# Kernel optimization log

Measured on AMD Instinct MI355X. Metric: run time of the kernel, lower is better.

The kernel has to match this reference:

```python
import jax, jax.numpy as jnp
import numpy as np

N_NODES = 50000
D_IN = 128
D_OUT = 128
E_POS = 500000
E_NEG = 100000
BN_EPS = 1e-5


def setup_inputs() -> dict:
    key = jax.random.key(0)
    k = jax.random.split(key, 4)
    x = jax.random.normal(k[0], (N_NODES, D_IN), dtype=jnp.float32)
    pos_edge_index = jax.random.randint(k[1], (2, E_POS), 0, N_NODES, dtype=jnp.int64)
    neg_edge_index = jax.random.randint(k[2], (2, E_NEG), 0, N_NODES, dtype=jnp.int64)
    W = jax.random.normal(k[3], (D_IN, D_OUT), dtype=jnp.float32) * 0.05
    b = jnp.zeros((D_OUT,), dtype=jnp.float32)
    gamma = jnp.ones((D_OUT,), dtype=jnp.float32)
    beta = jnp.zeros((D_OUT,), dtype=jnp.float32)
    return {"x": x, "pos_edge_index": pos_edge_index, "neg_edge_index": neg_edge_index,
            "W": W, "b": b, "gamma": gamma, "beta": beta}


def reference(x, pos_edge_index, neg_edge_index, W, b, gamma, beta):
    N = x.shape[0]
    # edge weights: 1 for pos edges, 0 for neg edges (as in the torch module)
    ei = jnp.concatenate([pos_edge_index, neg_edge_index], axis=1)
    w = jnp.concatenate([jnp.ones((pos_edge_index.shape[1],), x.dtype),
                         jnp.zeros((neg_edge_index.shape[1],), x.dtype)])
    # GCNConv gcn_norm: add self-loops with weight 1.0
    loop = jnp.arange(N)
    row = jnp.concatenate([ei[0], loop])
    col = jnp.concatenate([ei[1], loop])
    w = jnp.concatenate([w, jnp.ones((N,), x.dtype)])
    # symmetric degree normalization over target (col)
    deg = jax.ops.segment_sum(w, col, num_segments=N)
    dis = jnp.where(deg > 0, jax.lax.rsqrt(jnp.maximum(deg, 1e-12)), 0.0)
    norm = dis[row] * w * dis[col]  # [E_total]
    # linear transform first, then scatter-add aggregation at col
    h = x @ W  # [N, D_OUT]
    out = jax.ops.segment_sum(norm[:, None] * h[row], col, num_segments=N) + b
    # BatchNorm1d (training mode, biased batch var) + ReLU
    mean = out.mean(axis=0)
    var = out.var(axis=0)
    xhat = (out - mean) * jax.lax.rsqrt(var + BN_EPS)
    return jax.nn.relu(gamma * xhat + beta)
```

## Files before the change

### kernel.cpp

```cpp
#include <hip/hip_runtime.h>

#define D 128
#define BN_EPS 1e-5f
#define K_ELL 40
#define NB_AGG 1024

typedef __attribute__((ext_vector_type(8))) short bf16x8;
typedef __attribute__((ext_vector_type(4))) float f32x4;

__device__ __forceinline__ unsigned bf16rne(float f) {
    unsigned u = __float_as_uint(f);
    return (u + 0x7fffu + ((u >> 16) & 1u)) >> 16;
}
__device__ __forceinline__ float bflo(unsigned p) { return __uint_as_float(p << 16); }
__device__ __forceinline__ float bfhi(unsigned p) { return __uint_as_float(p & 0xffff0000u); }

__global__ void prep(const int* __restrict__ prow, const int* __restrict__ pcol,
                     int* __restrict__ deg, int* __restrict__ ell,
                     int2* __restrict__ ovf, int* __restrict__ ovf_cnt,
                     const float* __restrict__ W, ushort* __restrict__ wbT, int E) {
    int gtid = blockIdx.x * blockDim.x + threadIdx.x;
    int gsz = gridDim.x * blockDim.x;
    for (int i = gtid; i < D * D; i += gsz) {
        int k = i >> 7, c = i & 127;
        wbT[c * D + k] = (ushort)bf16rne(W[i]);
    }
    for (int e = gtid; e < E; e += gsz) {
        int c = pcol[e];
        int r = prow[e];
        int p = atomicAdd(&deg[c], 1);
        if (p < K_ELL) {
            ell[c * K_ELL + p] = r;
        } else {
            int q = atomicAdd(ovf_cnt, 1);
            ovf[q] = make_int2(c, r);
        }
    }
}

__global__ __launch_bounds__(256) void gemm_mfma(const float* __restrict__ x,
                                                 const ushort* __restrict__ wbT,
                                                 ushort* __restrict__ hb, int n) {
    __shared__ ushort xsb[64][136];
    __shared__ ushort wsb[128][136];
    int tid = threadIdx.x;
    int wave = tid >> 6;
    int lane = tid & 63;
    int row0 = blockIdx.x * 64;

    #pragma unroll
    for (int i = 0; i < 8; i++) {
        int flat = i * 256 + tid;
        int c = flat >> 4, seg = flat & 15;
        *(uint4*)&wsb[c][seg * 8] = ((const uint4*)wbT)[flat];
    }
    {
        int r = tid >> 2, kq = tid & 3;
        int grow = row0 + r;
        if (grow >= n) grow = n - 1;
        const float4* src = (const float4*)&x[(size_t)grow * D + kq * 32];
        uint* dst = (uint*)&xsb[r][kq * 32];
        #pragma unroll
        for (int q = 0; q < 8; q++) {
            float4 v = src[q];
            dst[q * 2]     = bf16rne(v.x) | (bf16rne(v.y) << 16);
            dst[q * 2 + 1] = bf16rne(v.z) | (bf16rne(v.w) << 16);
        }
    }
    __syncthreads();

    f32x4 acc[4][2];
    #pragma unroll
    for (int mt = 0; mt < 4; mt++)
        #pragma unroll
        for (int nt = 0; nt < 2; nt++)
            acc[mt][nt] = (f32x4){0.f, 0.f, 0.f, 0.f};

    int ar = lane & 15;
    int ako = (lane >> 4) * 8;
    #pragma unroll
    for (int k0 = 0; k0 < 128; k0 += 32) {
        bf16x8 a[4], b[2];
        #pragma unroll
        for (int mt = 0; mt < 4; mt++)
            a[mt] = *(const bf16x8*)&xsb[mt * 16 + ar][k0 + ako];
        #pragma unroll
        for (int nt = 0; nt < 2; nt++)
            b[nt] = *(const bf16x8*)&wsb[wave * 32 + nt * 16 + ar][k0 + ako];
        #pragma unroll
        for (int mt = 0; mt < 4; mt++)
            #pragma unroll
            for (int nt = 0; nt < 2; nt++)
                acc[mt][nt] = __builtin_amdgcn_mfma_f32_16x16x32_bf16(
                    a[mt], b[nt], acc[mt][nt], 0, 0, 0);
    }

    int col = lane & 15, rq = (lane >> 4) * 4;
    #pragma unroll
    for (int mt = 0; mt < 4; mt++) {
        #pragma unroll
        for (int r = 0; r < 4; r++) {
            int grow = row0 + mt * 16 + rq + r;
            if (grow < n) {
                #pragma unroll
                for (int nt = 0; nt < 2; nt++)
                    hb[(size_t)grow * D + wave * 32 + nt * 16 + col] =
                        (ushort)bf16rne(acc[mt][nt][r]);
            }
        }
    }
}

__global__ __launch_bounds__(512) void aggregate(const unsigned* __restrict__ hb,
                                                 const int* __restrict__ deg,
                                                 const int* __restrict__ ell,
                                                 const int2* __restrict__ ovf,
                                                 const int* __restrict__ ovf_cnt,
                                                 const float* __restrict__ bias,
                                                 float* __restrict__ out,
                                                 float* __restrict__ partials, int n) {
    int tid = threadIdx.x;
    int wave = tid >> 6;
    int lane = tid & 63;
    float2 bv = *(const float2*)&bias[lane * 2];
    float s1a = 0.f, s1b = 0.f, s2a = 0.f, s2b = 0.f;

    for (int node = blockIdx.x * 8 + wave; node < n; node += gridDim.x * 8) {
        int cntT = deg[node];
        float dc = rsqrtf((float)cntT + 1.0f);
        int cntE = cntT < K_ELL ? cntT : K_ELL;
        unsigned hp = hb[(size_t)node * 64 + lane];
        float ax = dc * bflo(hp), ay = dc * bfhi(hp);
        int es = (lane < cntE) ? ell[node * K_ELL + lane] : 0;
        float ed = (lane < cntE) ? rsqrtf((float)deg[es] + 1.0f) : 0.f;
        int e = 0;
        for (; e + 4 <= cntE; e += 4) {
            int sA = __shfl(es, e), sB = __shfl(es, e + 1);
            int sC = __shfl(es, e + 2), sD = __shfl(es, e + 3);
            float dA = __shfl(ed, e), dB = __shfl(ed, e + 1);
            float dC = __shfl(ed, e + 2), dD = __shfl(ed, e + 3);
            unsigned hA = hb[(size_t)sA * 64 + lane];
            unsigned hB = hb[(size_t)sB * 64 + lane];
            unsigned hC = hb[(size_t)sC * 64 + lane];
            unsigned hD = hb[(size_t)sD * 64 + lane];
            ax += dA * bflo(hA); ay += dA * bfhi(hA);
            ax += dB * bflo(hB); ay += dB * bfhi(hB);
            ax += dC * bflo(hC); ay += dC * bfhi(hC);
            ax += dD * bflo(hD); ay += dD * bfhi(hD);
        }
        for (; e < cntE; e++) {
            int s = __shfl(es, e);
            float dv = __shfl(ed, e);
            unsigned hq = hb[(size_t)s * 64 + lane];
            ax += dv * bflo(hq); ay += dv * bfhi(hq);
        }
        if (cntT > K_ELL) {
            int novf = *ovf_cnt;
            for (int j = 0; j < novf; j++) {
                int2 q = ovf[j];
                if (q.x == node) {
                    float dv = rsqrtf((float)deg[q.y] + 1.0f);
                    unsigned hq = hb[(size_t)q.y * 64 + lane];
                    ax += dv * bflo(hq); ay += dv * bfhi(hq);
                }
            }
        }
        float ox = dc * ax + bv.x;
        float oy = dc * ay + bv.y;
        *(float2*)&out[(size_t)node * D + lane * 2] = make_float2(ox, oy);
        s1a += ox; s1b += oy;
        s2a += ox * ox; s2b += oy * oy;
    }

    __shared__ float l1[8][128], l2[8][128];
    l1[wave][lane * 2] = s1a; l1[wave][lane * 2 + 1] = s1b;
    l2[wave][lane * 2] = s2a; l2[wave][lane * 2 + 1] = s2b;
    __syncthreads();
    if (tid < 256) {
        int col = tid & 127;
        float v;
        if (tid < 128) {
            v = l1[0][col] + l1[1][col] + l1[2][col] + l1[3][col] +
                l1[4][col] + l1[5][col] + l1[6][col] + l1[7][col];
        } else {
            v = l2[0][col] + l2[1][col] + l2[2][col] + l2[3][col] +
                l2[4][col] + l2[5][col] + l2[6][col] + l2[7][col];
        }
        partials[(size_t)blockIdx.x * 256 + tid] = v;
    }
}

__global__ __launch_bounds__(256) void bn_reduce(const float* __restrict__ partials,
                                                 float* __restrict__ gsum,
                                                 float* __restrict__ gsumsq, int nrows) {
    int tid = threadIdx.x;
    float s = 0.f;
    for (int r = blockIdx.x; r < nrows; r += gridDim.x)
        s += partials[(size_t)r * 256 + tid];
    if (tid < 128) atomicAdd(&gsum[tid], s);
    else           atomicAdd(&gsumsq[tid - 128], s);
}

__global__ __launch_bounds__(256) void bn_finalize(float4* __restrict__ out4,
                                                   const float* __restrict__ gsum,
                                                   const float* __restrict__ gsumsq,
                                                   const float* __restrict__ gamma,
                                                   const float* __restrict__ beta,
                                                   int total4, float invN) {
    int i0 = blockIdx.x * 256 + threadIdx.x;
    int c = (i0 * 4) & 127;
    float4 g4 = *(const float4*)&gsum[c];
    float4 q4 = *(const float4*)&gsumsq[c];
    float4 gm = *(const float4*)&gamma[c];
    float4 bt = *(const float4*)&beta[c];
    float m0 = g4.x * invN, m1 = g4.y * invN, m2 = g4.z * invN, m3 = g4.w * invN;
    float sc0 = rsqrtf(q4.x * invN - m0 * m0 + BN_EPS) * gm.x;
    float sc1 = rsqrtf(q4.y * invN - m1 * m1 + BN_EPS) * gm.y;
    float sc2 = rsqrtf(q4.z * invN - m2 * m2 + BN_EPS) * gm.z;
    float sc3 = rsqrtf(q4.w * invN - m3 * m3 + BN_EPS) * gm.w;
    float sh0 = bt.x - m0 * sc0, sh1 = bt.y - m1 * sc1;
    float sh2 = bt.z - m2 * sc2, sh3 = bt.w - m3 * sc3;
    for (int i = i0; i < total4; i += gridDim.x * 256) {
        float4 v = out4[i];
        v.x = fmaxf(fmaf(v.x, sc0, sh0), 0.f);
        v.y = fmaxf(fmaf(v.y, sc1, sh1), 0.f);
        v.z = fmaxf(fmaf(v.z, sc2, sh2), 0.f);
        v.w = fmaxf(fmaf(v.w, sc3, sh3), 0.f);
        out4[i] = v;
    }
}

extern "C" void kernel_launch(void* const* d_in, const int* in_sizes, int n_in,
                              void* d_out, int out_size, void* d_ws, size_t ws_size,
                              hipStream_t stream) {
    const float* x     = (const float*)d_in[0];
    const int*   pos   = (const int*)d_in[1];
    const float* W     = (const float*)d_in[3];
    const float* bias  = (const float*)d_in[4];
    const float* gamma = (const float*)d_in[5];
    const float* beta  = (const float*)d_in[6];
    float* out = (float*)d_out;

    int N  = in_sizes[0] / D;
    int EP = in_sizes[1] / 2;
    const int* prow = pos;
    const int* pcol = pos + EP;

    auto align = [](size_t v) { return (v + 255) & ~(size_t)255; };
    char* p = (char*)d_ws;
    int*      deg     = (int*)p;      p += align((size_t)N * 4);
    int*      ovf_cnt = (int*)p;      p += align(256);
    float*    gsum    = (float*)p;    p += align((size_t)D * 4);
    float*    gsumsq  = (float*)p;    p += align((size_t)D * 4);
    size_t zbytes = (size_t)(p - (char*)d_ws);
    ushort*   wbT      = (ushort*)p;   p += align((size_t)D * D * 2);
    int*      ell      = (int*)p;      p += align((size_t)N * K_ELL * 4);
    int2*     ovf      = (int2*)p;     p += align((size_t)EP * 8);
    ushort*   hb       = (ushort*)p;   p += align((size_t)N * D * 2);
    float*    partials = (float*)p;    p += align((size_t)NB_AGG * 256 * 4);

    hipMemsetAsync(d_ws, 0, zbytes, stream);
    prep<<<(EP + 255) / 256, 256, 0, stream>>>(prow, pcol, deg, ell, ovf, ovf_cnt,
                                               W, wbT, EP);
    gemm_mfma<<<(N + 63) / 64, 256, 0, stream>>>(x, wbT, hb, N);
    aggregate<<<NB_AGG, 512, 0, stream>>>((const unsigned*)hb, deg, ell, ovf, ovf_cnt,
                                          bias, out, partials, N);
    bn_reduce<<<64, 256, 0, stream>>>(partials, gsum, gsumsq, NB_AGG);
    bn_finalize<<<1600, 256, 0, stream>>>((float4*)out, gsum, gsumsq, gamma, beta,
                                          N * D / 4, 1.0f / (float)N);
}
```

Before: 158.7 us.

## Fuse GEMM with ELL fill, process two nodes per wave, fold BN reduce into aggregate

Merges the edge-bucketing prep kernel into the GEMM launch as extra blocks, so the GEMM converts W to bf16 directly instead of reading a pre-transposed copy. Aggregation now handles two nodes per wave, using half-waves to hold neighbor lists and issuing eight gathers per iteration for more memory-level parallelism. The separate BN reduction kernel is replaced by a last-block ticket reduction inside aggregate that writes per-column scale and shift. This removes two launches and overlaps the GEMM with the atomic fill, at the cost of redundant W conversion per GEMM block and more divergence and register pressure in aggregation.

Result: slower. 570.4 us (+259.5%).

```diff
diff --git a/kernel.cpp b/kernel.cpp
--- a/kernel.cpp
+++ b/kernel.cpp
@@ -4,6 +4,7 @@
 #define BN_EPS 1e-5f
 #define K_ELL 40
 #define NB_AGG 1024
+#define NB_FILL 1024
 
 typedef __attribute__((ext_vector_type(8))) short bf16x8;
 typedef __attribute__((ext_vector_type(4))) float f32x4;
@@ -15,44 +16,47 @@
 __device__ __forceinline__ float bflo(unsigned p) { return __uint_as_float(p << 16); }
 __device__ __forceinline__ float bfhi(unsigned p) { return __uint_as_float(p & 0xffff0000u); }
 
-__global__ void prep(const int* __restrict__ prow, const int* __restrict__ pcol,
-                     int* __restrict__ deg, int* __restrict__ ell,
-                     int2* __restrict__ ovf, int* __restrict__ ovf_cnt,
-                     const float* __restrict__ W, ushort* __restrict__ wbT, int E) {
-    int gtid = blockIdx.x * blockDim.x + threadIdx.x;
-    int gsz = gridDim.x * blockDim.x;
-    for (int i = gtid; i < D * D; i += gsz) {
-        int k = i >> 7, c = i & 127;
-        wbT[c * D + k] = (ushort)bf16rne(W[i]);
-    }
-    for (int e = gtid; e < E; e += gsz) {
-        int c = pcol[e];
-        int r = prow[e];
-        int p = atomicAdd(&deg[c], 1);
-        if (p < K_ELL) {
-            ell[c * K_ELL + p] = r;
-        } else {
-            int q = atomicAdd(ovf_cnt, 1);
-            ovf[q] = make_int2(c, r);
-        }
-    }
-}
-
-__global__ __launch_bounds__(256) void gemm_mfma(const float* __restrict__ x,
-                                                 const ushort* __restrict__ wbT,
-                                                 ushort* __restrict__ hb, int n) {
+__global__ __launch_bounds__(256) void gemm_fill(
+    const float* __restrict__ x, const float* __restrict__ W,
+    const int* __restrict__ prow, const int* __restrict__ pcol,
+    int* __restrict__ deg, int* __restrict__ ell,
+    int2* __restrict__ ovf, int* __restrict__ ovf_cnt,
+    ushort* __restrict__ hb, int n, int E, int gemm_nb)
+{
     __shared__ ushort xsb[64][136];
     __shared__ ushort wsb[128][136];
     int tid = threadIdx.x;
+
+    if (blockIdx.x >= gemm_nb) {
+        int gtid = (blockIdx.x - gemm_nb) * 256 + tid;
+        for (int e = gtid; e < E; e += NB_FILL * 256) {
+            int c = pcol[e];
+            int r = prow[e];
+            int p = atomicAdd(&deg[c], 1);
+            if (p < K_ELL) {
+                ell[c * K_ELL + p] = r;
+            } else {
+                int q = atomicAdd(ovf_cnt, 1);
+                ovf[q] = make_int2(c, r);
+            }
+        }
+        return;
+    }
+
     int wave = tid >> 6;
     int lane = tid & 63;
     int row0 = blockIdx.x * 64;
 
     #pragma unroll
-    for (int i = 0; i < 8; i++) {
+    for (int i = 0; i < 16; i++) {
         int flat = i * 256 + tid;
-        int c = flat >> 4, seg = flat & 15;
-        *(uint4*)&wsb[c][seg * 8] = ((const uint4*)wbT)[flat];
+        int k = flat >> 5;
+        int c4 = flat & 31;
+        float4 v = *(const float4*)&W[k * D + c4 * 4];
+        wsb[c4 * 4 + 0][k] = (ushort)bf16rne(v.x);
+        wsb[c4 * 4 + 1][k] = (ushort)bf16rne(v.y);
+        wsb[c4 * 4 + 2][k] = (ushort)bf16rne(v.z);
+        wsb[c4 * 4 + 3][k] = (ushort)bf16rne(v.w);
     }
     {
         int r = tid >> 2, kq = tid & 3;
@@ -111,68 +115,108 @@
     }
 }
 
-__global__ __launch_bounds__(512) void aggregate(const unsigned* __restrict__ hb,
-                                                 const int* __restrict__ deg,
-                                                 const int* __restrict__ ell,
-                                                 const int2* __restrict__ ovf,
-                                                 const int* __restrict__ ovf_cnt,
-                                                 const float* __restrict__ bias,
-                                                 float* __restrict__ out,
-                                                 float* __restrict__ partials, int n) {
+__global__ __launch_bounds__(512) void aggregate(
+    const unsigned* __restrict__ hb, const int* __restrict__ deg,
+    const int* __restrict__ ell, const int2* __restrict__ ovf,
+    const int* __restrict__ ovf_cnt, const float* __restrict__ bias,
+    const float* __restrict__ gamma, const float* __restrict__ beta,
+    float* __restrict__ out, float* __restrict__ partials,
+    int* __restrict__ ticket, float* __restrict__ scs_g, float* __restrict__ shs_g,
+    int n, float invN)
+{
     int tid = threadIdx.x;
     int wave = tid >> 6;
     int lane = tid & 63;
+    int half = lane >> 5;
+    int sub = lane & 31;
     float2 bv = *(const float2*)&bias[lane * 2];
     float s1a = 0.f, s1b = 0.f, s2a = 0.f, s2b = 0.f;
 
-    for (int node = blockIdx.x * 8 + wave; node < n; node += gridDim.x * 8) {
-        int cntT = deg[node];
-        float dc = rsqrtf((float)cntT + 1.0f);
-        int cntE = cntT < K_ELL ? cntT : K_ELL;
-        unsigned hp = hb[(size_t)node * 64 + lane];
-        float ax = dc * bflo(hp), ay = dc * bfhi(hp);
-        int es = (lane < cntE) ? ell[node * K_ELL + lane] : 0;
-        float ed = (lane < cntE) ? rsqrtf((float)deg[es] + 1.0f) : 0.f;
-        int e = 0;
-        for (; e + 4 <= cntE; e += 4) {
-            int sA = __shfl(es, e), sB = __shfl(es, e + 1);
-            int sC = __shfl(es, e + 2), sD = __shfl(es, e + 3);
-            float dA = __shfl(ed, e), dB = __shfl(ed, e + 1);
-            float dC = __shfl(ed, e + 2), dD = __shfl(ed, e + 3);
-            unsigned hA = hb[(size_t)sA * 64 + lane];
-            unsigned hB = hb[(size_t)sB * 64 + lane];
-            unsigned hC = hb[(size_t)sC * 64 + lane];
-            unsigned hD = hb[(size_t)sD * 64 + lane];
-            ax += dA * bflo(hA); ay += dA * bfhi(hA);
-            ax += dB * bflo(hB); ay += dB * bfhi(hB);
-            ax += dC * bflo(hC); ay += dC * bfhi(hC);
-            ax += dD * bflo(hD); ay += dD * bfhi(hD);
-        }
-        for (; e < cntE; e++) {
-            int s = __shfl(es, e);
-            float dv = __shfl(ed, e);
+    for (int base = blockIdx.x * 16 + wave * 2; base < n; base += gridDim.x * 16) {
+        int n0 = base;
+        bool has1 = (base + 1 < n);
+        int n1 = has1 ? base + 1 : base;
+        int c0T = deg[n0];
+        int c1T = deg[n1];
+        float dc0 = rsqrtf((float)c0T + 1.0f);
+        float dc1 = rsqrtf((float)c1T + 1.0f);
+        unsigned hp0 = hb[(size_t)n0 * 64 + lane];
+        unsigned hp1 = hb[(size_t)n1 * 64 + lane];
+        float ax0 = dc0 * bflo(hp0), ay0 = dc0 * bfhi(hp0);
+        float ax1 = dc1 * bflo(hp1), ay1 = dc1 * bfhi(hp1);
+        int c0E = c0T < 32 ? c0T : 32;
+        int c1E = c1T < 32 ? c1T : 32;
+        if (!has1) c1E = 0;
+        int mynode = half ? n1 : n0;
+        int mycE = half ? c1E : c0E;
+        int es = (sub < mycE) ? ell[mynode * K_ELL + sub] : mynode;
+        float ed = (sub < mycE) ? rsqrtf((float)deg[es] + 1.0f) : 0.f;
+        int cap = c0E > c1E ? c0E : c1E;
+        int iters = (cap + 3) >> 2;
+        for (int it = 0; it < iters; it++) {
+            int e = it * 4;
+            int sa0 = __shfl(es, e),      sb0 = __shfl(es, e + 1);
+            int sc0i = __shfl(es, e + 2), sd0 = __shfl(es, e + 3);
+            int sa1 = __shfl(es, 32 + e),     sb1 = __shfl(es, 33 + e);
+            int sc1i = __shfl(es, 34 + e),    sd1 = __shfl(es, 35 + e);
+            float da0 = __shfl(ed, e),      db0 = __shfl(ed, e + 1);
+            float dc0w = __shfl(ed, e + 2), dd0 = __shfl(ed, e + 3);
+            float da1 = __shfl(ed, 32 + e),     db1 = __shfl(ed, 33 + e);
+            float dc1w = __shfl(ed, 34 + e),    dd1 = __shfl(ed, 35 + e);
+            unsigned ha0 = hb[(size_t)sa0 * 64 + lane];
+            unsigned hb0 = hb[(size_t)sb0 * 64 + lane];
+            unsigned hc0 = hb[(size_t)sc0i * 64 + lane];
+            unsigned hd0 = hb[(size_t)sd0 * 64 + lane];
+            unsigned ha1 = hb[(size_t)sa1 * 64 + lane];
+            unsigned hb1 = hb[(size_t)sb1 * 64 + lane];
+            unsigned hc1 = hb[(size_t)sc1i * 64 + lane];
+            unsigned hd1 = hb[(size_t)sd1 * 64 + lane];
+            ax0 += da0 * bflo(ha0);  ay0 += da0 * bfhi(ha0);
+            ax0 += db0 * bflo(hb0);  ay0 += db0 * bfhi(hb0);
+            ax0 += dc0w * bflo(hc0); ay0 += dc0w * bfhi(hc0);
+            ax0 += dd0 * bflo(hd0);  ay0 += dd0 * bfhi(hd0);
+            ax1 += da1 * bflo(ha1);  ay1 += da1 * bfhi(ha1);
+            ax1 += db1 * bflo(hb1);  ay1 += db1 * bfhi(hb1);
+            ax1 += dc1w * bflo(hc1); ay1 += dc1w * bfhi(hc1);
+            ax1 += dd1 * bflo(hd1);  ay1 += dd1 * bfhi(hd1);
+        }
+        for (int e = 32; e < c0T && e < K_ELL; e++) {
+            int s = ell[n0 * K_ELL + e];
+            float dv = rsqrtf((float)deg[s] + 1.0f);
             unsigned hq = hb[(size_t)s * 64 + lane];
-            ax += dv * bflo(hq); ay += dv * bfhi(hq);
-        }
-        if (cntT > K_ELL) {
+            ax0 += dv * bflo(hq); ay0 += dv * bfhi(hq);
+        }
+        if (has1) for (int e = 32; e < c1T && e < K_ELL; e++) {
+            int s = ell[n1 * K_ELL + e];
+            float dv = rsqrtf((float)deg[s] + 1.0f);
+            unsigned hq = hb[(size_t)s * 64 + lane];
+            ax1 += dv * bflo(hq); ay1 += dv * bfhi(hq);
+        }
+        if (c0T > K_ELL || (has1 && c1T > K_ELL)) {
             int novf = *ovf_cnt;
             for (int j = 0; j < novf; j++) {
                 int2 q = ovf[j];
-                if (q.x == node) {
-                    float dv = rsqrtf((float)deg[q.y] + 1.0f);
-                    unsigned hq = hb[(size_t)q.y * 64 + lane];
-                    ax += dv * bflo(hq); ay += dv * bfhi(hq);
-                }
+                float dv = rsqrtf((float)deg[q.y] + 1.0f);
+                unsigned hq = hb[(size_t)q.y * 64 + lane];
+                if (q.x == n0) { ax0 += dv * bflo(hq); ay0 += dv * bfhi(hq); }
+                if (has1 && q.x == n1) { ax1 += dv * bflo(hq); ay1 += dv * bfhi(hq); }
             }
         }
-        float ox = dc * ax + bv.x;
-        float oy = dc * ay + bv.y;
-        *(float2*)&out[(size_t)node * D + lane * 2] = make_float2(ox, oy);
-        s1a += ox; s1b += oy;
-        s2a += ox * ox; s2b += oy * oy;
+        float ox0 = dc0 * ax0 + bv.x;
+        float oy0 = dc0 * ay0 + bv.y;
+        *(float2*)&out[(size_t)n0 * D + lane * 2] = make_float2(ox0, oy0);
+        s1a += ox0; s1b += oy0; s2a += ox0 * ox0; s2b += oy0 * oy0;
+        if (has1) {
+            float ox1 = dc1 * ax1 + bv.x;
+            float oy1 = dc1 * ay1 + bv.y;
+            *(float2*)&out[(size_t)n1 * D + lane * 2] = make_float2(ox1, oy1);
+            s1a += ox1; s1b += oy1; s2a += ox1 * ox1; s2b += oy1 * oy1;
+        }
     }
 
     __shared__ float l1[8][128], l2[8][128];
+    __shared__ float stats[256];
+    __shared__ int amlast;
     l1[wave][lane * 2] = s1a; l1[wave][lane * 2 + 1] = s1b;
     l2[wave][lane * 2] = s2a; l2[wave][lane * 2 + 1] = s2b;
     __syncthreads();
@@ -188,44 +232,43 @@
         }
         partials[(size_t)blockIdx.x * 256 + tid] = v;
     }
-}
-
-__global__ __launch_bounds__(256) void bn_reduce(const float* __restrict__ partials,
-                                                 float* __restrict__ gsum,
-                                                 float* __restrict__ gsumsq, int nrows) {
-    int tid = threadIdx.x;
-    float s = 0.f;
-    for (int r = blockIdx.x; r < nrows; r += gridDim.x)
-        s += partials[(size_t)r * 256 + tid];
-    if (tid < 128) atomicAdd(&gsum[tid], s);
-    else           atomicAdd(&gsumsq[tid - 128], s);
+    __threadfence();
+    __syncthreads();
+    if (tid == 0) amlast = (atomicAdd(ticket, 1) == (int)gridDim.x - 1);
+    __syncthreads();
+    if (amlast) {
+        __threadfence();
+        if (tid < 256) {
+            float s = 0.f;
+            for (int r = 0; r < (int)gridDim.x; r++)
+                s += partials[(size_t)r * 256 + tid];
+            stats[tid] = s;
+        }
+        __syncthreads();
+        if (tid < 128) {
+            float m = stats[tid] * invN;
+            float var = stats[tid + 128] * invN - m * m;
+            float sc = rsqrtf(var + BN_EPS) * gamma[tid];
+            scs_g[tid] = sc;
+            shs_g[tid] = beta[tid] - m * sc;
+        }
+    }
 }
 
 __global__ __launch_bounds__(256) void bn_finalize(float4* __restrict__ out4,
-                                                   const float* __restrict__ gsum,
-                                                   const float* __restrict__ gsumsq,
-                                                   const float* __restrict__ gamma,
-                                                   const float* __restrict__ beta,
-                                                   int total4, float invN) {
+                                                   const float* __restrict__ scs,
+                                                   const float* __restrict__ shs,
+                                                   int total4) {
     int i0 = blockIdx.x * 256 + threadIdx.x;
     int c = (i0 * 4) & 127;
-    float4 g4 = *(const float4*)&gsum[c];
-    float4 q4 = *(const float4*)&gsumsq[c];
-    float4 gm = *(const float4*)&gamma[c];
-    float4 bt = *(const float4*)&beta[c];
-    float m0 = g4.x * invN, m1 = g4.y * invN, m2 = g4.z * invN, m3 = g4.w * invN;
-    float sc0 = rsqrtf(q4.x * invN - m0 * m0 + BN_EPS) * gm.x;
-    float sc1 = rsqrtf(q4.y * invN - m1 * m1 + BN_EPS) * gm.y;
-    float sc2 = rsqrtf(q4.z * invN - m2 * m2 + BN_EPS) * gm.z;
-    float sc3 = rsqrtf(q4.w * invN - m3 * m3 + BN_EPS) * gm.w;
-    float sh0 = bt.x - m0 * sc0, sh1 = bt.y - m1 * sc1;
-    float sh2 = bt.z - m2 * sc2, sh3 = bt.w - m3 * sc3;
+    float4 sc = *(const float4*)&scs[c];
+    float4 sh = *(const float4*)&shs[c];
     for (int i = i0; i < total4; i += gridDim.x * 256) {
         float4 v = out4[i];
-        v.x = fmaxf(fmaf(v.x, sc0, sh0), 0.f);
-        v.y = fmaxf(fmaf(v.y, sc1, sh1), 0.f);
-        v.z = fmaxf(fmaf(v.z, sc2, sh2), 0.f);
-        v.w = fmaxf(fmaf(v.w, sc3, sh3), 0.f);
+        v.x = fmaxf(fmaf(v.x, sc.x, sh.x), 0.f);
+        v.y = fmaxf(fmaf(v.y, sc.y, sh.y), 0.f);
+        v.z = fmaxf(fmaf(v.z, sc.z, sh.z), 0.f);
+        v.w = fmaxf(fmaf(v.w, sc.w, sh.w), 0.f);
         out4[i] = v;
     }
 }
@@ -245,27 +288,26 @@
     int EP = in_sizes[1] / 2;
     const int* prow = pos;
     const int* pcol = pos + EP;
+    int gemm_nb = (N + 63) / 64;
 
     auto align = [](size_t v) { return (v + 255) & ~(size_t)255; };
     char* p = (char*)d_ws;
-    int*      deg     = (int*)p;      p += align((size_t)N * 4);
-    int*      ovf_cnt = (int*)p;      p += align(256);
-    float*    gsum    = (float*)p;    p += align((size_t)D * 4);
-    float*    gsumsq  = (float*)p;    p += align((size_t)D * 4);
+    int*    deg     = (int*)p;    p += align((size_t)N * 4);
+    int*    ovf_cnt = (int*)p;    p += align(256);
+    int*    ticket  = (int*)p;    p += align(256);
     size_t zbytes = (size_t)(p - (char*)d_ws);
-    ushort*   wbT      = (ushort*)p;   p += align((size_t)D * D * 2);
-    int*      ell      = (int*)p;      p += align((size_t)N * K_ELL * 4);
-    int2*     ovf      = (int2*)p;     p += align((size_t)EP * 8);
-    ushort*   hb       = (ushort*)p;   p += align((size_t)N * D * 2);
-    float*    partials = (float*)p;    p += align((size_t)NB_AGG * 256 * 4);
+    int*    ell      = (int*)p;    p += align((size_t)N * K_ELL * 4);
+    int2*   ovf      = (int2*)p;   p += align((size_t)EP * 8);
+    ushort* hb       = (ushort*)p; p += align((size_t)N * D * 2);
+    float*  partials = (float*)p;  p += align((size_t)NB_AGG * 256 * 4);
+    float*  scs      = (float*)p;  p += align((size_t)D * 4);
+    float*  shs      = (float*)p;  p += align((size_t)D * 4);
 
     hipMemsetAsync(d_ws, 0, zbytes, stream);
-    prep<<<(EP + 255) / 256, 256, 0, stream>>>(prow, pcol, deg, ell, ovf, ovf_cnt,
-                                               W, wbT, EP);
-    gemm_mfma<<<(N + 63) / 64, 256, 0, stream>>>(x, wbT, hb, N);
+    gemm_fill<<<gemm_nb + NB_FILL, 256, 0, stream>>>(x, W, prow, pcol, deg, ell, ovf,
+                                                     ovf_cnt, hb, N, EP, gemm_nb);
     aggregate<<<NB_AGG, 512, 0, stream>>>((const unsigned*)hb, deg, ell, ovf, ovf_cnt,
-                                          bias, out, partials, N);
-    bn_reduce<<<64, 256, 0, stream>>>(partials, gsum, gsumsq, NB_AGG);
-    bn_finalize<<<1600, 256, 0, stream>>>((float4*)out, gsum, gsumsq, gamma, beta,
-                                          N * D / 4, 1.0f / (float)N);
-}
+                                          bias, gamma, beta, out, partials, ticket,
+                                          scs, shs, N, 1.0f / (float)N);
+    bn_finalize<<<1600, 256, 0, stream>>>((float4*)out, scs, shs, N * D / 4);
+}
```

## Fuse ELL fill and bf16 GEMM into one launch with block specialization

Applied to the files above, without the earlier changes.

Merges the edge-bucketing prep kernel and the MFMA GEMM kernel into a single launch, where the first blocks do the GEMM and the extra blocks do the atomic ELL fill in a grid-stride loop. Each GEMM block now converts and transposes W to bf16 in shared memory itself, so the separate wbT buffer and its pass go away. This removes one kernel launch boundary and lets the atomic-bound fill overlap with the compute-bound GEMM. In exchange, the W transpose is redone in every GEMM block, and its strided 2-byte shared-memory stores may hit bank conflicts.

Result: slower. 164.1 us (+3.4%).

```diff
diff --git a/kernel.cpp b/kernel.cpp
--- a/kernel.cpp
+++ b/kernel.cpp
@@ -4,6 +4,7 @@
 #define BN_EPS 1e-5f
 #define K_ELL 40
 #define NB_AGG 1024
+#define NB_FILL 1024
 
 typedef __attribute__((ext_vector_type(8))) short bf16x8;
 typedef __attribute__((ext_vector_type(4))) float f32x4;
@@ -15,44 +16,47 @@
 __device__ __forceinline__ float bflo(unsigned p) { return __uint_as_float(p << 16); }
 __device__ __forceinline__ float bfhi(unsigned p) { return __uint_as_float(p & 0xffff0000u); }
 
-__global__ void prep(const int* __restrict__ prow, const int* __restrict__ pcol,
-                     int* __restrict__ deg, int* __restrict__ ell,
-                     int2* __restrict__ ovf, int* __restrict__ ovf_cnt,
-                     const float* __restrict__ W, ushort* __restrict__ wbT, int E) {
-    int gtid = blockIdx.x * blockDim.x + threadIdx.x;
-    int gsz = gridDim.x * blockDim.x;
-    for (int i = gtid; i < D * D; i += gsz) {
-        int k = i >> 7, c = i & 127;
-        wbT[c * D + k] = (ushort)bf16rne(W[i]);
-    }
-    for (int e = gtid; e < E; e += gsz) {
-        int c = pcol[e];
-        int r = prow[e];
-        int p = atomicAdd(&deg[c], 1);
-        if (p < K_ELL) {
-            ell[c * K_ELL + p] = r;
-        } else {
-            int q = atomicAdd(ovf_cnt, 1);
-            ovf[q] = make_int2(c, r);
-        }
-    }
-}
-
-__global__ __launch_bounds__(256) void gemm_mfma(const float* __restrict__ x,
-                                                 const ushort* __restrict__ wbT,
-                                                 ushort* __restrict__ hb, int n) {
+__global__ __launch_bounds__(256) void gemm_fill(
+    const float* __restrict__ x, const float* __restrict__ W,
+    const int* __restrict__ prow, const int* __restrict__ pcol,
+    int* __restrict__ deg, int* __restrict__ ell,
+    int2* __restrict__ ovf, int* __restrict__ ovf_cnt,
+    ushort* __restrict__ hb, int n, int E, int gemm_nb)
+{
     __shared__ ushort xsb[64][136];
     __shared__ ushort wsb[128][136];
     int tid = threadIdx.x;
+
+    if (blockIdx.x >= gemm_nb) {
+        int gtid = (blockIdx.x - gemm_nb) * 256 + tid;
+        for (int e = gtid; e < E; e += NB_FILL * 256) {
+            int c = pcol[e];
+            int r = prow[e];
+            int p = atomicAdd(&deg[c], 1);
+            if (p < K_ELL) {
+                ell[c * K_ELL + p] = r;
+            } else {
+                int q = atomicAdd(ovf_cnt, 1);
+                ovf[q] = make_int2(c, r);
+            }
+        }
+        return;
+    }
+
     int wave = tid >> 6;
     int lane = tid & 63;
     int row0 = blockIdx.x * 64;
 
     #pragma unroll
-    for (int i = 0; i < 8; i++) {
+    for (int i = 0; i < 16; i++) {
         int flat = i * 256 + tid;
-        int c = flat >> 4, seg = flat & 15;
-        *(uint4*)&wsb[c][seg * 8] = ((const uint4*)wbT)[flat];
+        int k = flat >> 5;
+        int c4 = flat & 31;
+        float4 v = *(const float4*)&W[k * D + c4 * 4];
+        wsb[c4 * 4 + 0][k] = (ushort)bf16rne(v.x);
+        wsb[c4 * 4 + 1][k] = (ushort)bf16rne(v.y);
+        wsb[c4 * 4 + 2][k] = (ushort)bf16rne(v.z);
+        wsb[c4 * 4 + 3][k] = (ushort)bf16rne(v.w);
     }
     {
         int r = tid >> 2, kq = tid & 3;
@@ -245,24 +249,23 @@
     int EP = in_sizes[1] / 2;
     const int* prow = pos;
     const int* pcol = pos + EP;
+    int gemm_nb = (N + 63) / 64;
 
     auto align = [](size_t v) { return (v + 255) & ~(size_t)255; };
     char* p = (char*)d_ws;
-    int*      deg     = (int*)p;      p += align((size_t)N * 4);
-    int*      ovf_cnt = (int*)p;      p += align(256);
-    float*    gsum    = (float*)p;    p += align((size_t)D * 4);
-    float*    gsumsq  = (float*)p;    p += align((size_t)D * 4);
+    int*    deg     = (int*)p;    p += align((size_t)N * 4);
+    int*    ovf_cnt = (int*)p;    p += align(256);
+    float*  gsum    = (float*)p;  p += align((size_t)D * 4);
+    float*  gsumsq  = (float*)p;  p += align((size_t)D * 4);
     size_t zbytes = (size_t)(p - (char*)d_ws);
-    ushort*   wbT      = (ushort*)p;   p += align((size_t)D * D * 2);
-    int*      ell      = (int*)p;      p += align((size_t)N * K_ELL * 4);
-    int2*     ovf      = (int2*)p;     p += align((size_t)EP * 8);
-    ushort*   hb       = (ushort*)p;   p += align((size_t)N * D * 2);
-    float*    partials = (float*)p;    p += align((size_t)NB_AGG * 256 * 4);
+    int*    ell      = (int*)p;    p += align((size_t)N * K_ELL * 4);
+    int2*   ovf      = (int2*)p;   p += align((size_t)EP * 8);
+    ushort* hb       = (ushort*)p; p += align((size_t)N * D * 2);
+    float*  partials = (float*)p;  p += align((size_t)NB_AGG * 256 * 4);
 
     hipMemsetAsync(d_ws, 0, zbytes, stream);
-    prep<<<(EP + 255) / 256, 256, 0, stream>>>(prow, pcol, deg, ell, ovf, ovf_cnt,
-                                               W, wbT, EP);
-    gemm_mfma<<<(N + 63) / 64, 256, 0, stream>>>(x, wbT, hb, N);
+    gemm_fill<<<gemm_nb + NB_FILL, 256, 0, stream>>>(x, W, prow, pcol, deg, ell, ovf,
+                                                     ovf_cnt, hb, N, EP, gemm_nb);
     aggregate<<<NB_AGG, 512, 0, stream>>>((const unsigned*)hb, deg, ell, ovf, ovf_cnt,
                                           bias, out, partials, N);
     bn_reduce<<<64, 256, 0, stream>>>(partials, gsum, gsumsq, NB_AGG);
```
